# Kernel tuning notes

Measured on AMD Instinct MI355X. Metric: run time of the kernel, lower is better.

The kernel has to match this reference:

```python
import math
import jax, jax.numpy as jnp
import numpy as np

N = 50000          # nodes
E = 1_600_000      # edges
DNE = 128
DED = 128
NUM_RBF = 50
R_CUT = 5.0
LN_EPS = 1e-5


def setup_inputs() -> dict:
    key = jax.random.key(0)
    ks = jax.random.split(key, 16)
    z = jax.random.normal(ks[0], (N, 25), jnp.float32)
    edge = jax.random.randint(ks[1], (E, 2), 0, N, dtype=jnp.int64)
    r = jax.random.uniform(ks[2], (E,), jnp.float32) * (R_CUT * 1.1)  # some beyond cutoff
    u_raw = jax.random.normal(ks[3], (E, 3), jnp.float32)
    u = u_raw / jnp.linalg.norm(u_raw, axis=-1, keepdims=True)

    def xavier(k, shape):
        fan_in, fan_out = shape
        lim = math.sqrt(6.0 / (fan_in + fan_out))
        return jax.random.uniform(k, shape, jnp.float32, -lim, lim)

    return {
        "z": z, "edge": edge, "r": r, "u": u,
        "A_na_w": xavier(ks[4], (25, DNE)), "A_na_b": jnp.zeros((DNE,), jnp.float32),
        "A_nbr_w": xavier(ks[5], (25, DNE)), "A_nbr_b": jnp.zeros((DNE,), jnp.float32),
        "W_ndp_w": xavier(ks[6], (NUM_RBF, DNE)), "W_ndp_b": jnp.zeros((DNE,), jnp.float32),
        "W_nrd_w": xavier(ks[7], (2 * DNE, DNE)), "W_nrd_b": jnp.zeros((DNE,), jnp.float32),
        "W_nru_w": xavier(ks[8], (DNE, DNE)), "W_nru_b": jnp.zeros((DNE,), jnp.float32),
        "W_erp_w": xavier(ks[9], (NUM_RBF, DED)), "W_erp_b": jnp.zeros((DED,), jnp.float32),
        "ln_g": jnp.ones((DNE,), jnp.float32), "ln_b": jnp.zeros((DNE,), jnp.float32),
    }


def _sh_l2(u):
    x, y, zc = u[:, 0], u[:, 1], u[:, 2]
    s3 = math.sqrt(3.0)
    return jnp.stack([
        s3 * x * y,
        s3 * y * zc,
        0.5 * (3.0 * zc * zc - 1.0),
        s3 * zc * x,
        0.5 * s3 * (x * x - y * y),
    ], axis=-1)  # [E, 5]


def _rbf(r):
    start = math.exp(-R_CUT)
    means = jnp.linspace(start, 1.0, NUM_RBF)
    beta = (2.0 / NUM_RBF * (1.0 - start)) ** (-2)
    alpha = 5.0 / R_CUT
    return jnp.exp(-beta * (jnp.exp(-alpha * r[:, None]) - means) ** 2)  # [E, NUM_RBF]


def reference(z, edge, r, u,
              A_na_w, A_na_b, A_nbr_w, A_nbr_b,
              W_ndp_w, W_ndp_b, W_nrd_w, W_nrd_b,
              W_nru_w, W_nru_b, W_erp_w, W_erp_b,
              ln_g, ln_b):
    i, j = edge[:, 0], edge[:, 1]
    n_nodes = z.shape[0]

    # edge tensor representations (Lmax=2)
    rt0 = r[:, None]          # [E,1]
    rt1 = u                   # [E,3]
    rt2 = _sh_l2(u)           # [E,5]

    rbf = _rbf(r)                                              # [E,R]
    c = (0.5 * (jnp.cos(math.pi * r / R_CUT) + 1.0)
         * (r < R_CUT).astype(r.dtype))[:, None]               # [E,1]

    nbr = jax.nn.silu(z @ A_nbr_w + A_nbr_b)                   # [N,dne]
    gate = (rbf @ W_ndp_w + W_ndp_b) * c                       # [E,dne]
    msg = nbr[j] * gate                                        # gather + gate
    m = jax.ops.segment_sum(msg, i, num_segments=n_nodes)      # scatter-add [N,dne]

    na = jax.nn.silu(z @ A_na_w + A_na_b)
    h = jnp.concatenate([na, m], axis=-1) @ W_nrd_w + W_nrd_b  # [N,dne]
    mu = jnp.mean(h, axis=-1, keepdims=True)
    var = jnp.var(h, axis=-1, keepdims=True)
    h = (h - mu) / jnp.sqrt(var + LN_EPS) * ln_g + ln_b
    h = jax.nn.silu(h)
    h = h @ W_nru_w + W_nru_b                                  # [N,dne]

    t = (h[i] + h[j]) * (rbf @ W_erp_w + W_erp_b)              # [E,ded]
    return (h, t, rt0, rt1, rt2, c)
```

## Files before the change

kernel.cpp:

```cpp
#include <hip/hip_runtime.h>
#include <hip/hip_bf16.h>
#include <math.h>

#define NN 50000
#define NE 1600000
#define D 128
#define NRBF 50
#define RCUT 5.0f
#define LNEPS 1e-5f
#define EB 16
#define EB2 64
#define EDGE_GRID 2048
#define SCAN_B 196
#define NB 16
#define NPB 8

typedef __attribute__((ext_vector_type(8))) short bf16x8;
typedef __attribute__((ext_vector_type(4))) float f32x4;

__device__ __forceinline__ float silu_f(float x) {
    return x / (1.0f + __expf(-x));
}
__device__ __forceinline__ unsigned short f2bf(float x) {
    __hip_bfloat16 b = __float2bfloat16(x);
    return *reinterpret_cast<unsigned short*>(&b);
}
__device__ __forceinline__ float bf2f(unsigned short u) {
    unsigned int x = ((unsigned int)u) << 16;
    return __uint_as_float(x);
}

__global__ __launch_bounds__(128) void nbr_kernel(
    const float* __restrict__ z, const float* __restrict__ Aw,
    const float* __restrict__ Ab, unsigned short* __restrict__ nbr_bf)
{
    const int n = blockIdx.x;
    const int d = threadIdx.x;
    float acc = Ab[d];
#pragma unroll
    for (int k = 0; k < 25; ++k)
        acc = fmaf(z[n * 25 + k], Aw[k * D + d], acc);
    nbr_bf[(size_t)n * D + d] = f2bf(silu_f(acc));
}

__global__ __launch_bounds__(256) void aux_kernel(
    const int* __restrict__ edge, const float* __restrict__ r,
    const float* __restrict__ u, float* __restrict__ rt0,
    float* __restrict__ rt1, float* __restrict__ rt2,
    float* __restrict__ cout, int* __restrict__ cnt)
{
    const int e = blockIdx.x * 256 + threadIdx.x;
    if (e >= NE) return;
    const float rr = r[e];
    rt0[e] = rr;
    const float cc = (rr < RCUT)
        ? 0.5f * (__cosf(3.14159265358979f * rr * (1.0f / RCUT)) + 1.0f)
        : 0.0f;
    cout[e] = cc;
    const float x  = u[e * 3 + 0];
    const float y  = u[e * 3 + 1];
    const float zc = u[e * 3 + 2];
    rt1[(size_t)e * 3 + 0] = x;
    rt1[(size_t)e * 3 + 1] = y;
    rt1[(size_t)e * 3 + 2] = zc;
    const float s3 = 1.7320508075688772f;
    rt2[(size_t)e * 5 + 0] = s3 * x * y;
    rt2[(size_t)e * 5 + 1] = s3 * y * zc;
    rt2[(size_t)e * 5 + 2] = 0.5f * (3.0f * zc * zc - 1.0f);
    rt2[(size_t)e * 5 + 3] = s3 * zc * x;
    rt2[(size_t)e * 5 + 4] = 0.5f * s3 * (x * x - y * y);
    atomicAdd(&cnt[edge[2 * e]], 1);
}

__global__ __launch_bounds__(256) void scan1_kernel(
    const int* __restrict__ cnt, int* __restrict__ off, int* __restrict__ bsum)
{
    __shared__ int s[2][256];
    const int t = threadIdx.x;
    const int g = blockIdx.x * 256 + t;
    const int v = (g < NN) ? cnt[g] : 0;
    int incl = v;
    s[0][t] = incl;
    __syncthreads();
    int cur = 0;
#pragma unroll
    for (int dd = 1; dd < 256; dd <<= 1) {
        const int add = (t >= dd) ? s[cur][t - dd] : 0;
        incl += add;
        s[cur ^ 1][t] = incl;
        __syncthreads();
        cur ^= 1;
    }
    if (g < NN) off[g] = incl - v;
    if (t == 255) bsum[blockIdx.x] = incl;
}

__global__ __launch_bounds__(256) void scan2_kernel(int* __restrict__ bsum)
{
    __shared__ int s[2][256];
    const int t = threadIdx.x;
    const int v = (t < SCAN_B) ? bsum[t] : 0;
    int incl = v;
    s[0][t] = incl;
    __syncthreads();
    int cur = 0;
#pragma unroll
    for (int dd = 1; dd < 256; dd <<= 1) {
        const int add = (t >= dd) ? s[cur][t - dd] : 0;
        incl += add;
        s[cur ^ 1][t] = incl;
        __syncthreads();
        cur ^= 1;
    }
    if (t < SCAN_B) bsum[t] = incl - v;
}

__global__ __launch_bounds__(256) void scan3_kernel(
    int* __restrict__ off, const int* __restrict__ bsum)
{
    const int g = blockIdx.x * 256 + threadIdx.x;
    if (g < NN) off[g] += bsum[blockIdx.x];
    if (g == 0) off[NN] = NE;
}

__global__ __launch_bounds__(256) void scatter_kernel(
    const int* __restrict__ edge, const int* __restrict__ off,
    int* __restrict__ cursor, int* __restrict__ elist)
{
    const int e = blockIdx.x * 256 + threadIdx.x;
    if (e >= NE) return;
    const int i = edge[2 * e];
    const int pos = atomicAdd(&cursor[i], 1);
    elist[off[i] + pos] = e;
}

__global__ __launch_bounds__(128) void gather_msg_mfma(
    const int* __restrict__ elist, const int* __restrict__ off,
    const int* __restrict__ edge, const float* __restrict__ r,
    const float* __restrict__ W_ndp, const float* __restrict__ b_ndp,
    const unsigned short* __restrict__ nbr_bf, float* __restrict__ m)
{
    __shared__ unsigned short P[EB][64];
    __shared__ float er_s[EB];
    __shared__ float c_s[EB];
    __shared__ int   j_s[EB];

    const int tid = threadIdx.x;
    const int w   = tid >> 6;
    const int l   = tid & 63;
    const int lr  = l & 15;
    const int lg  = l >> 4;

    bf16x8 wf[4][2];
#pragma unroll
    for (int dt = 0; dt < 4; ++dt) {
        const int col = w * 64 + dt * 16 + lr;
#pragma unroll
        for (int s = 0; s < 2; ++s) {
            bf16x8 v;
#pragma unroll
            for (int j = 0; j < 8; ++j) {
                const int k = s * 32 + lg * 8 + j;
                float wv = 0.0f;
                if (k < NRBF)       wv = W_ndp[k * D + col];
                else if (k == NRBF) wv = b_ndp[col];
                v[j] = (short)f2bf(wv);
            }
            wf[dt][s] = v;
        }
    }

    const float start = expf(-RCUT);
    const float step  = (1.0f - start) / (NRBF - 1);
    const float bq    = (2.0f / NRBF) * (1.0f - start);
    const float beta  = 1.0f / (bq * bq);

    const int prow = tid >> 3;
    const int pci  = tid & 7;

    for (int nn = 0; nn < NPB; ++nn) {
        const int n   = blockIdx.x * NPB + nn;
        const int s0  = off[n];
        const int deg = off[n + 1] - s0;

        f32x4 macc[4] = {{0,0,0,0},{0,0,0,0},{0,0,0,0},{0,0,0,0}};

        for (int base = 0; base < deg; base += EB) {
            const int chunk = min(EB, deg - base);
            if (tid < EB) {
                if (tid < chunk) {
                    const int eid = elist[s0 + base + tid];
                    const float rr = r[eid];
                    er_s[tid] = __expf(-rr);
                    c_s[tid] = (rr < RCUT)
                        ? 0.5f * (__cosf(3.14159265358979f * rr * (1.0f / RCUT)) + 1.0f)
                        : 0.0f;
                    j_s[tid] = edge[2 * eid + 1];
                } else {
                    er_s[tid] = 0.0f; c_s[tid] = 0.0f; j_s[tid] = 0;
                }
            }
            __syncthreads();
            {
                const float er = er_s[prow];
                const float cc = c_s[prow];
                unsigned int pk[4];
#pragma unroll
                for (int p2 = 0; p2 < 4; ++p2) {
                    unsigned int word = 0;
#pragma unroll
                    for (int c = 0; c < 2; ++c) {
                        const int k = pci * 8 + p2 * 2 + c;
                        float v = 0.0f;
                        if (k < NRBF) {
                            const float diff = er - (start + (float)k * step);
                            v = cc * __expf(-beta * diff * diff);
                        } else if (k == NRBF) {
                            v = cc;
                        }
                        word |= ((unsigned int)f2bf(v)) << (16 * c);
                    }
                    pk[p2] = word;
                }
                const int swc = pci ^ (prow & 7);
                *(uint4*)&P[prow][swc * 8] = make_uint4(pk[0], pk[1], pk[2], pk[3]);
            }
            __syncthreads();
            bf16x8 af[2];
#pragma unroll
            for (int s = 0; s < 2; ++s) {
                const int swc = (s * 4 + lg) ^ (lr & 7);
                af[s] = *(const bf16x8*)&P[lr][swc * 8];
            }
            int jrow[4];
#pragma unroll
            for (int q = 0; q < 4; ++q) jrow[q] = j_s[lg * 4 + q];
#pragma unroll
            for (int dt = 0; dt < 4; ++dt) {
                f32x4 acc = {0.0f, 0.0f, 0.0f, 0.0f};
                acc = __builtin_amdgcn_mfma_f32_16x16x32_bf16(af[0], wf[dt][0], acc, 0, 0, 0);
                acc = __builtin_amdgcn_mfma_f32_16x16x32_bf16(af[1], wf[dt][1], acc, 0, 0, 0);
                const int col = w * 64 + dt * 16 + lr;
#pragma unroll
                for (int q = 0; q < 4; ++q) {
                    const float nv = bf2f(nbr_bf[(size_t)jrow[q] * D + col]);
                    macc[dt][q] = fmaf(nv, acc[q], macc[dt][q]);
                }
            }
            __syncthreads();
        }

#pragma unroll
        for (int dt = 0; dt < 4; ++dt) {
            float v = macc[dt][0] + macc[dt][1] + macc[dt][2] + macc[dt][3];
            v += __shfl_xor(v, 16);
            v += __shfl_xor(v, 32);
            if (lg == 0)
                m[(size_t)n * D + w * 64 + dt * 16 + lr] = v;
        }
    }
}

__global__ __launch_bounds__(256) void node_kernel2(
    const float* __restrict__ z, const float* __restrict__ A_na_w,
    const float* __restrict__ A_na_b, const float* __restrict__ m,
    const float* __restrict__ W_nrd_w, const float* __restrict__ W_nrd_b,
    const float* __restrict__ W_nru_w, const float* __restrict__ W_nru_b,
    const float* __restrict__ ln_g, const float* __restrict__ ln_b,
    float* __restrict__ hout, unsigned short* __restrict__ h_bf)
{
    __shared__ float inbuf[NB][260];
    __shared__ float wbuf[32][128];
    __shared__ float part[4][NB][2];

    const int tid = threadIdx.x;
    const int n0 = blockIdx.x * NB;
    const int nl = tid & 15;
    const int dg = tid >> 4;

    for (int idx = tid; idx < NB * 128; idx += 256) {
        const int n = idx >> 7;
        const int d = idx & 127;
        float acc = A_na_b[d];
#pragma unroll
        for (int k = 0; k < 25; ++k)
            acc = fmaf(z[(size_t)(n0 + n) * 25 + k], A_na_w[k * D + d], acc);
        inbuf[n][d]       = silu_f(acc);
        inbuf[n][128 + d] = m[(size_t)(n0 + n) * D + d];
    }

    float h1[8];
#pragma unroll
    for (int dd = 0; dd < 8; ++dd) h1[dd] = W_nrd_b[dg * 8 + dd];

    for (int tile = 0; tile < 8; ++tile) {
        __syncthreads();
        for (int v = tid; v < 32 * 32; v += 256) {
            const int row = v >> 5;
            const int c4  = (v & 31) * 4;
            *(float4*)&wbuf[row][c4] =
                *(const float4*)&W_nrd_w[(size_t)(tile * 32 + row) * D + c4];
        }
        __syncthreads();
#pragma unroll 4
        for (int k = 0; k < 32; ++k) {
            const float rin = inbuf[nl][tile * 32 + k];
            const float4 wa = *(const float4*)&wbuf[k][dg * 8];
            const float4 wb = *(const float4*)&wbuf[k][dg * 8 + 4];
            h1[0] = fmaf(rin, wa.x, h1[0]);
            h1[1] = fmaf(rin, wa.y, h1[1]);
            h1[2] = fmaf(rin, wa.z, h1[2]);
            h1[3] = fmaf(rin, wa.w, h1[3]);
            h1[4] = fmaf(rin, wb.x, h1[4]);
            h1[5] = fmaf(rin, wb.y, h1[5]);
            h1[6] = fmaf(rin, wb.z, h1[6]);
            h1[7] = fmaf(rin, wb.w, h1[7]);
        }
    }

    float s = 0.0f, sq = 0.0f;
#pragma unroll
    for (int dd = 0; dd < 8; ++dd) { s += h1[dd]; sq += h1[dd] * h1[dd]; }
    s  += __shfl_xor(s, 16);  sq += __shfl_xor(sq, 16);
    s  += __shfl_xor(s, 32);  sq += __shfl_xor(sq, 32);
    const int wv = tid >> 6;
    if ((tid & 63) < 16) { part[wv][nl][0] = s; part[wv][nl][1] = sq; }
    __syncthreads();
    float ts = 0.0f, tsq = 0.0f;
#pragma unroll
    for (int w = 0; w < 4; ++w) { ts += part[w][nl][0]; tsq += part[w][nl][1]; }
    const float mu  = ts * (1.0f / 128.0f);
    const float var = tsq * (1.0f / 128.0f) - mu * mu;
    const float inv = rsqrtf(var + LNEPS);

#pragma unroll
    for (int dd = 0; dd < 8; ++dd) {
        const int d = dg * 8 + dd;
        inbuf[nl][d] = silu_f((h1[dd] - mu) * inv * ln_g[d] + ln_b[d]);
    }

    float h2[8];
#pragma unroll
    for (int dd = 0; dd < 8; ++dd) h2[dd] = W_nru_b[dg * 8 + dd];

    for (int tile = 0; tile < 4; ++tile) {
        __syncthreads();
        for (int v = tid; v < 32 * 32; v += 256) {
            const int row = v >> 5;
            const int c4  = (v & 31) * 4;
            *(float4*)&wbuf[row][c4] =
                *(const float4*)&W_nru_w[(size_t)(tile * 32 + row) * D + c4];
        }
        __syncthreads();
#pragma unroll 4
        for (int k = 0; k < 32; ++k) {
            const float rin = inbuf[nl][tile * 32 + k];
            const float4 wa = *(const float4*)&wbuf[k][dg * 8];
            const float4 wb = *(const float4*)&wbuf[k][dg * 8 + 4];
            h2[0] = fmaf(rin, wa.x, h2[0]);
            h2[1] = fmaf(rin, wa.y, h2[1]);
            h2[2] = fmaf(rin, wa.z, h2[2]);
            h2[3] = fmaf(rin, wa.w, h2[3]);
            h2[4] = fmaf(rin, wb.x, h2[4]);
            h2[5] = fmaf(rin, wb.y, h2[5]);
            h2[6] = fmaf(rin, wb.z, h2[6]);
            h2[7] = fmaf(rin, wb.w, h2[7]);
        }
    }

    float4 o0 = {h2[0], h2[1], h2[2], h2[3]};
    float4 o1 = {h2[4], h2[5], h2[6], h2[7]};
    *(float4*)&hout[(size_t)(n0 + nl) * D + dg * 8]     = o0;
    *(float4*)&hout[(size_t)(n0 + nl) * D + dg * 8 + 4] = o1;

    unsigned int b0 = (unsigned int)f2bf(h2[0]) | ((unsigned int)f2bf(h2[1]) << 16);
    unsigned int b1 = (unsigned int)f2bf(h2[2]) | ((unsigned int)f2bf(h2[3]) << 16);
    unsigned int b2 = (unsigned int)f2bf(h2[4]) | ((unsigned int)f2bf(h2[5]) << 16);
    unsigned int b3 = (unsigned int)f2bf(h2[6]) | ((unsigned int)f2bf(h2[7]) << 16);
    *(uint4*)&h_bf[(size_t)(n0 + nl) * D + dg * 8] = make_uint4(b0, b1, b2, b3);
}

__global__ __launch_bounds__(256) void edge_out_mfma(
    const int* __restrict__ edge, const float* __restrict__ r,
    const float* __restrict__ W_erp, const float* __restrict__ b_erp,
    const unsigned short* __restrict__ h_bf, float* __restrict__ t)
{
    __shared__ unsigned short P[EB2][64];
    __shared__ unsigned short hv[EB2][136];
    __shared__ int ij_s[EB2][2];

    const int tid = threadIdx.x;
    const int w  = tid >> 6;
    const int l  = tid & 63;
    const int lr = l & 15;
    const int lg = l >> 4;

    bf16x8 wf[8][2];
    float bias[8];
#pragma unroll
    for (int dt = 0; dt < 8; ++dt) {
        const int col = dt * 16 + lr;
        bias[dt] = b_erp[col];
#pragma unroll
        for (int s = 0; s < 2; ++s) {
            bf16x8 v;
#pragma unroll
            for (int j = 0; j < 8; ++j) {
                const int k = s * 32 + lg * 8 + j;
                v[j] = (k < NRBF) ? (short)f2bf(W_erp[k * D + col]) : (short)0;
            }
            wf[dt][s] = v;
        }
    }

    const float start = expf(-RCUT);
    const float step  = (1.0f - start) / (NRBF - 1);
    const float bq    = (2.0f / NRBF) * (1.0f - start);
    const float beta  = 1.0f / (bq * bq);

    const int prow  = tid & 63;
    const int kbase = (tid >> 6) * 16;

    const int nbatch = NE / EB2;
    for (int batch = blockIdx.x; batch < nbatch; batch += gridDim.x) {
        const int eb = batch * EB2;
        if (tid < EB2) {
            const int2 ep = ((const int2*)edge)[eb + tid];
            ij_s[tid][0] = ep.x;
            ij_s[tid][1] = ep.y;
        }
        {
            const float er = __expf(-r[eb + prow]);
            const int kc0 = kbase >> 3;
#pragma unroll
            for (int c2 = 0; c2 < 2; ++c2) {
                const int kc = kc0 + c2;
                unsigned int pk[4];
#pragma unroll
                for (int p2 = 0; p2 < 4; ++p2) {
                    unsigned int word = 0;
#pragma unroll
                    for (int c = 0; c < 2; ++c) {
                        const int k = kc * 8 + p2 * 2 + c;
                        float v = 0.0f;
                        if (k < NRBF) {
                            const float diff = er - (start + (float)k * step);
                            v = __expf(-beta * diff * diff);
                        }
                        word |= ((unsigned int)f2bf(v)) << (16 * c);
                    }
                    pk[p2] = word;
                }
                const int swc = kc ^ (prow & 7);
                *(uint4*)&P[prow][swc * 8] = make_uint4(pk[0], pk[1], pk[2], pk[3]);
            }
        }
        __syncthreads();

        const int arow = w * 16 + lr;
        bf16x8 af[2];
#pragma unroll
        for (int s = 0; s < 2; ++s) {
            const int swc = (s * 4 + lg) ^ (arow & 7);
            af[s] = *(const bf16x8*)&P[arow][swc * 8];
        }

#pragma unroll
        for (int idx = tid; idx < EB2 * 16; idx += 256) {
            const int el = idx >> 4;
            const int ch = idx & 15;
            const uint4 ui = *((const uint4*)(h_bf + (size_t)ij_s[el][0] * D) + ch);
            const uint4 uj = *((const uint4*)(h_bf + (size_t)ij_s[el][1] * D) + ch);
            const unsigned int wi[4] = {ui.x, ui.y, ui.z, ui.w};
            const unsigned int wj[4] = {uj.x, uj.y, uj.z, uj.w};
            unsigned int wo[4];
#pragma unroll
            for (int p = 0; p < 4; ++p) {
                const float lo = bf2f((unsigned short)(wi[p] & 0xffff))
                               + bf2f((unsigned short)(wj[p] & 0xffff));
                const float hi = bf2f((unsigned short)(wi[p] >> 16))
                               + bf2f((unsigned short)(wj[p] >> 16));
                wo[p] = (unsigned int)f2bf(lo) | ((unsigned int)f2bf(hi) << 16);
            }
            *(uint4*)&hv[el][ch * 8] = make_uint4(wo[0], wo[1], wo[2], wo[3]);
        }
        __syncthreads();

#pragma unroll
        for (int dt = 0; dt < 8; ++dt) {
            f32x4 acc = {0.0f, 0.0f, 0.0f, 0.0f};
            acc = __builtin_amdgcn_mfma_f32_16x16x32_bf16(af[0], wf[dt][0], acc, 0, 0, 0);
            acc = __builtin_amdgcn_mfma_f32_16x16x32_bf16(af[1], wf[dt][1], acc, 0, 0, 0);
            const int col = dt * 16 + lr;
#pragma unroll
            for (int q = 0; q < 4; ++q) {
                const int el = w * 16 + lg * 4 + q;
                const float hvf = bf2f(hv[el][col]);
                t[(size_t)(eb + el) * D + col] = hvf * (acc[q] + bias[dt]);
            }
        }
        __syncthreads();
    }
}

extern "C" void kernel_launch(void* const* d_in, const int* in_sizes, int n_in,
                              void* d_out, int out_size, void* d_ws, size_t ws_size,
                              hipStream_t stream) {
    const float* z      = (const float*)d_in[0];
    const int*   edge   = (const int*)d_in[1];
    const float* r      = (const float*)d_in[2];
    const float* u      = (const float*)d_in[3];
    const float* A_na_w  = (const float*)d_in[4];
    const float* A_na_b  = (const float*)d_in[5];
    const float* A_nbr_w = (const float*)d_in[6];
    const float* A_nbr_b = (const float*)d_in[7];
    const float* W_ndp_w = (const float*)d_in[8];
    const float* W_ndp_b = (const float*)d_in[9];
    const float* W_nrd_w = (const float*)d_in[10];
    const float* W_nrd_b = (const float*)d_in[11];
    const float* W_nru_w = (const float*)d_in[12];
    const float* W_nru_b = (const float*)d_in[13];
    const float* W_erp_w = (const float*)d_in[14];
    const float* W_erp_b = (const float*)d_in[15];
    const float* ln_g    = (const float*)d_in[16];
    const float* ln_b    = (const float*)d_in[17];

    float* out = (float*)d_out;
    float* h_out   = out;
    float* t_out   = out + (size_t)NN * D;
    float* rt0_out = t_out + (size_t)NE * D;
    float* rt1_out = rt0_out + (size_t)NE;
    float* rt2_out = rt1_out + (size_t)NE * 3;
    float* c_out   = rt2_out + (size_t)NE * 5;

    unsigned short* nbr_bf = (unsigned short*)d_ws;
    float* m_ws   = (float*)((char*)d_ws + (size_t)NN * D * sizeof(unsigned short));
    unsigned short* h_bf = (unsigned short*)((char*)m_ws + (size_t)NN * D * sizeof(float));

    int* elist  = (int*)t_out;
    int* off    = elist + NE;
    int* cursor = off + (NN + 1);
    int* bsum   = cursor + NN;

    hipMemsetAsync(cursor, 0, (size_t)NN * sizeof(int), stream);

    nbr_kernel<<<NN, 128, 0, stream>>>(z, A_nbr_w, A_nbr_b, nbr_bf);

    aux_kernel<<<(NE + 255) / 256, 256, 0, stream>>>(
        edge, r, u, rt0_out, rt1_out, rt2_out, c_out, cursor);

    scan1_kernel<<<SCAN_B, 256, 0, stream>>>(cursor, off, bsum);
    scan2_kernel<<<1, 256, 0, stream>>>(bsum);
    scan3_kernel<<<SCAN_B, 256, 0, stream>>>(off, bsum);

    hipMemsetAsync(cursor, 0, (size_t)NN * sizeof(int), stream);

    scatter_kernel<<<(NE + 255) / 256, 256, 0, stream>>>(edge, off, cursor, elist);

    gather_msg_mfma<<<NN / NPB, 128, 0, stream>>>(
        elist, off, edge, r, W_ndp_w, W_ndp_b, nbr_bf, m_ws);

    node_kernel2<<<NN / NB, 256, 0, stream>>>(
        z, A_na_w, A_na_b, m_ws, W_nrd_w, W_nrd_b,
        W_nru_w, W_nru_b, ln_g, ln_b, h_out, h_bf);

    edge_out_mfma<<<EDGE_GRID, 256, 0, stream>>>(
        edge, r, W_erp_w, W_erp_b, h_bf, t_out);
}
```

Baseline: 850.1 us.

## Pack neighbor index and distance in CSR, vectorize gathers and output stores

The scatter step now writes (j, r) pairs into the CSR list, so the message kernel no longer does dependent random loads of edge and r through an edge id. The MFMA output columns are remapped (col = lr*4+dt and lr*8+dt) so each lane owns contiguous columns. That lets the nbr gather use 8-byte vector loads and the m and t writes use float4 stores instead of scalar strided accesses. In exchange the CSR scratch doubles in size and there is more register pressure from holding all accumulators before the epilogue.

```diff
diff --git a/kernel.cpp b/kernel.cpp
--- a/kernel.cpp
+++ b/kernel.cpp
@@ -124,19 +124,22 @@
 }
 
 __global__ __launch_bounds__(256) void scatter_kernel(
-    const int* __restrict__ edge, const int* __restrict__ off,
-    int* __restrict__ cursor, int* __restrict__ elist)
+    const int* __restrict__ edge, const float* __restrict__ r,
+    const int* __restrict__ off, int* __restrict__ cursor,
+    uint2* __restrict__ jr)
 {
     const int e = blockIdx.x * 256 + threadIdx.x;
     if (e >= NE) return;
-    const int i = edge[2 * e];
-    const int pos = atomicAdd(&cursor[i], 1);
-    elist[off[i] + pos] = e;
+    const int2 ep = ((const int2*)edge)[e];
+    const int pos = atomicAdd(&cursor[ep.x], 1);
+    uint2 v;
+    v.x = (unsigned int)ep.y;
+    v.y = __float_as_uint(r[e]);
+    jr[off[ep.x] + pos] = v;
 }
 
 __global__ __launch_bounds__(128) void gather_msg_mfma(
-    const int* __restrict__ elist, const int* __restrict__ off,
-    const int* __restrict__ edge, const float* __restrict__ r,
+    const uint2* __restrict__ jr, const int* __restrict__ off,
     const float* __restrict__ W_ndp, const float* __restrict__ b_ndp,
     const unsigned short* __restrict__ nbr_bf, float* __restrict__ m)
 {
@@ -154,7 +157,7 @@
     bf16x8 wf[4][2];
 #pragma unroll
     for (int dt = 0; dt < 4; ++dt) {
-        const int col = w * 64 + dt * 16 + lr;
+        const int col = w * 64 + lr * 4 + dt;
 #pragma unroll
         for (int s = 0; s < 2; ++s) {
             bf16x8 v;
@@ -189,13 +192,13 @@
             const int chunk = min(EB, deg - base);
             if (tid < EB) {
                 if (tid < chunk) {
-                    const int eid = elist[s0 + base + tid];
-                    const float rr = r[eid];
+                    const uint2 v = jr[s0 + base + tid];
+                    const float rr = __uint_as_float(v.y);
                     er_s[tid] = __expf(-rr);
                     c_s[tid] = (rr < RCUT)
                         ? 0.5f * (__cosf(3.14159265358979f * rr * (1.0f / RCUT)) + 1.0f)
                         : 0.0f;
-                    j_s[tid] = edge[2 * eid + 1];
+                    j_s[tid] = (int)v.x;
                 } else {
                     er_s[tid] = 0.0f; c_s[tid] = 0.0f; j_s[tid] = 0;
                 }
@@ -232,31 +235,41 @@
                 const int swc = (s * 4 + lg) ^ (lr & 7);
                 af[s] = *(const bf16x8*)&P[lr][swc * 8];
             }
-            int jrow[4];
-#pragma unroll
-            for (int q = 0; q < 4; ++q) jrow[q] = j_s[lg * 4 + q];
+            f32x4 accs[4];
 #pragma unroll
             for (int dt = 0; dt < 4; ++dt) {
                 f32x4 acc = {0.0f, 0.0f, 0.0f, 0.0f};
                 acc = __builtin_amdgcn_mfma_f32_16x16x32_bf16(af[0], wf[dt][0], acc, 0, 0, 0);
                 acc = __builtin_amdgcn_mfma_f32_16x16x32_bf16(af[1], wf[dt][1], acc, 0, 0, 0);
-                const int col = w * 64 + dt * 16 + lr;
-#pragma unroll
-                for (int q = 0; q < 4; ++q) {
-                    const float nv = bf2f(nbr_bf[(size_t)jrow[q] * D + col]);
-                    macc[dt][q] = fmaf(nv, acc[q], macc[dt][q]);
-                }
+                accs[dt] = acc;
+            }
+#pragma unroll
+            for (int q = 0; q < 4; ++q) {
+                const int row = j_s[lg * 4 + q];
+                const uint2 nv8 = *(const uint2*)(nbr_bf + (size_t)row * D + w * 64 + lr * 4);
+                const float n0 = bf2f((unsigned short)(nv8.x & 0xffff));
+                const float n1 = bf2f((unsigned short)(nv8.x >> 16));
+                const float n2 = bf2f((unsigned short)(nv8.y & 0xffff));
+                const float n3 = bf2f((unsigned short)(nv8.y >> 16));
+                macc[0][q] = fmaf(n0, accs[0][q], macc[0][q]);
+                macc[1][q] = fmaf(n1, accs[1][q], macc[1][q]);
+                macc[2][q] = fmaf(n2, accs[2][q], macc[2][q]);
+                macc[3][q] = fmaf(n3, accs[3][q], macc[3][q]);
             }
             __syncthreads();
         }
 
-#pragma unroll
-        for (int dt = 0; dt < 4; ++dt) {
-            float v = macc[dt][0] + macc[dt][1] + macc[dt][2] + macc[dt][3];
-            v += __shfl_xor(v, 16);
-            v += __shfl_xor(v, 32);
-            if (lg == 0)
-                m[(size_t)n * D + w * 64 + dt * 16 + lr] = v;
+        float v0 = macc[0][0] + macc[0][1] + macc[0][2] + macc[0][3];
+        float v1 = macc[1][0] + macc[1][1] + macc[1][2] + macc[1][3];
+        float v2 = macc[2][0] + macc[2][1] + macc[2][2] + macc[2][3];
+        float v3 = macc[3][0] + macc[3][1] + macc[3][2] + macc[3][3];
+        v0 += __shfl_xor(v0, 16); v0 += __shfl_xor(v0, 32);
+        v1 += __shfl_xor(v1, 16); v1 += __shfl_xor(v1, 32);
+        v2 += __shfl_xor(v2, 16); v2 += __shfl_xor(v2, 32);
+        v3 += __shfl_xor(v3, 16); v3 += __shfl_xor(v3, 32);
+        if (lg == 0) {
+            float4 o = {v0, v1, v2, v3};
+            *(float4*)&m[(size_t)n * D + w * 64 + lr * 4] = o;
         }
     }
 }
@@ -399,7 +412,7 @@
     float bias[8];
 #pragma unroll
     for (int dt = 0; dt < 8; ++dt) {
-        const int col = dt * 16 + lr;
+        const int col = lr * 8 + dt;
         bias[dt] = b_erp[col];
 #pragma unroll
         for (int s = 0; s < 2; ++s) {
@@ -486,18 +499,27 @@
         }
         __syncthreads();
 
+        f32x4 accs[8];
 #pragma unroll
         for (int dt = 0; dt < 8; ++dt) {
             f32x4 acc = {0.0f, 0.0f, 0.0f, 0.0f};
             acc = __builtin_amdgcn_mfma_f32_16x16x32_bf16(af[0], wf[dt][0], acc, 0, 0, 0);
             acc = __builtin_amdgcn_mfma_f32_16x16x32_bf16(af[1], wf[dt][1], acc, 0, 0, 0);
-            const int col = dt * 16 + lr;
-#pragma unroll
-            for (int q = 0; q < 4; ++q) {
-                const int el = w * 16 + lg * 4 + q;
-                const float hvf = bf2f(hv[el][col]);
-                t[(size_t)(eb + el) * D + col] = hvf * (acc[q] + bias[dt]);
-            }
+            accs[dt] = acc;
+        }
+#pragma unroll
+        for (int q = 0; q < 4; ++q) {
+            const int el = w * 16 + lg * 4 + q;
+            const bf16x8 hv8 = *(const bf16x8*)&hv[el][lr * 8];
+            float o[8];
+#pragma unroll
+            for (int dt = 0; dt < 8; ++dt)
+                o[dt] = bf2f((unsigned short)hv8[dt]) * (accs[dt][q] + bias[dt]);
+            float4 o0 = {o[0], o[1], o[2], o[3]};
+            float4 o1 = {o[4], o[5], o[6], o[7]};
+            float* tp = &t[(size_t)(eb + el) * D + lr * 8];
+            *(float4*)tp       = o0;
+            *(float4*)(tp + 4) = o1;
         }
         __syncthreads();
     }
@@ -537,8 +559,8 @@
     float* m_ws   = (float*)((char*)d_ws + (size_t)NN * D * sizeof(unsigned short));
     unsigned short* h_bf = (unsigned short*)((char*)m_ws + (size_t)NN * D * sizeof(float));
 
-    int* elist  = (int*)t_out;
-    int* off    = elist + NE;
+    uint2* jr   = (uint2*)t_out;
+    int* off    = (int*)(jr + NE);
     int* cursor = off + (NN + 1);
     int* bsum   = cursor + NN;
 
@@ -555,10 +577,10 @@
 
     hipMemsetAsync(cursor, 0, (size_t)NN * sizeof(int), stream);
 
-    scatter_kernel<<<(NE + 255) / 256, 256, 0, stream>>>(edge, off, cursor, elist);
+    scatter_kernel<<<(NE + 255) / 256, 256, 0, stream>>>(edge, r, off, cursor, jr);
 
     gather_msg_mfma<<<NN / NPB, 128, 0, stream>>>(
-        elist, off, edge, r, W_ndp_w, W_ndp_b, nbr_bf, m_ws);
+        jr, off, W_ndp_w, W_ndp_b, nbr_bf, m_ws);
 
     node_kernel2<<<NN / NB, 256, 0, stream>>>(
         z, A_na_w, A_na_b, m_ws, W_nrd_w, W_nrd_b,
```

After: 846.0 us. No clear change (-0.5%).
